# Kernel tuning notes

Hardware: AMD Instinct MI355X
Metric: run time of the kernel (lower is better)

The kernel has to match this reference:

```python
import jax, jax.numpy as jnp
import numpy as np

N_NODES = 20000
N_EDGES = 640000
NF = 128   # node_features
EF = 32    # edge_features
HD = 128   # hidden_dim
NL = 3     # num_layers
EPS = 1e-5


def _p(key, shape, scale=0.05):
    return scale * jax.random.normal(key, shape, dtype=jnp.float32)


def setup_inputs() -> dict:
    key = jax.random.key(0)
    ks = jax.random.split(key, 24)
    inp = {
        "node_coords": jax.random.normal(ks[0], (N_NODES, 6), dtype=jnp.float32),
        "edge_index": jax.random.randint(ks[1], (2, N_EDGES), 0, N_NODES, dtype=jnp.int64),
        "edge_distances": jax.random.normal(ks[2], (N_EDGES, 32), dtype=jnp.float32),
        # embeddings
        "W_node": _p(ks[3], (6, NF)), "b_node": jnp.zeros((NF,), jnp.float32),
        "W_edge": _p(ks[4], (32, EF)), "b_edge": jnp.zeros((EF,), jnp.float32),
        # stacked per-layer MPNN params [NL, ...]
        "msg_W1": _p(ks[5], (NL, 2 * NF + EF, HD)), "msg_b1": jnp.zeros((NL, HD), jnp.float32),
        "msg_W2": _p(ks[6], (NL, HD, HD)), "msg_b2": jnp.zeros((NL, HD), jnp.float32),
        "upd_W1": _p(ks[7], (NL, NF + HD, HD)), "upd_b1": jnp.zeros((NL, HD), jnp.float32),
        "upd_W2": _p(ks[8], (NL, HD, NF)), "upd_b2": jnp.zeros((NL, NF), jnp.float32),
        "ln_g": jnp.ones((NL, NF), jnp.float32), "ln_b": jnp.zeros((NL, NF), jnp.float32),
        # output projection
        "W_out": _p(ks[9], (NF, HD)), "b_out": jnp.zeros((HD,), jnp.float32),
    }
    return inp


def _layer_norm(x, g, b):
    mu = jnp.mean(x, axis=-1, keepdims=True)
    var = jnp.var(x, axis=-1, keepdims=True)
    return (x - mu) * jax.lax.rsqrt(var + EPS) * g + b


def _encode(node_coords, edge_index, edge_distances,
            W_node, b_node, W_edge, b_edge,
            msg_W1, msg_b1, msg_W2, msg_b2,
            upd_W1, upd_b1, upd_W2, upd_b2,
            ln_g, ln_b, W_out, b_out):
    src, dst = edge_index[0], edge_index[1]
    h = node_coords @ W_node + b_node                      # [N, NF]
    e = edge_distances @ W_edge + b_edge                   # [E, EF]
    n = h.shape[0]
    for l in range(NL):
        # gather + message MLP
        m_in = jnp.concatenate([h[src], h[dst], e], axis=-1)           # [E, 2NF+EF]
        m = jax.nn.relu(m_in @ msg_W1[l] + msg_b1[l]) @ msg_W2[l] + msg_b2[l]  # [E, HD]
        # scatter_add over destination nodes
        agg = jax.ops.segment_sum(m, dst, num_segments=n)              # [N, HD]
        # update MLP + residual + LayerNorm
        u_in = jnp.concatenate([h, agg], axis=-1)                      # [N, NF+HD]
        delta = jax.nn.relu(u_in @ upd_W1[l] + upd_b1[l]) @ upd_W2[l] + upd_b2[l]
        h = _layer_norm(h + delta, ln_g[l], ln_b[l])
    return h @ W_out + b_out                                           # [N, HD]


def reference(node_coords, edge_index, edge_distances,
              W_node, b_node, W_edge, b_edge,
              msg_W1, msg_b1, msg_W2, msg_b2,
              upd_W1, upd_b1, upd_W2, upd_b2,
              ln_g, ln_b, W_out, b_out):
    return _encode(node_coords, edge_index, edge_distances,
                   W_node, b_node, W_edge, b_edge,
                   msg_W1, msg_b1, msg_W2, msg_b2,
                   upd_W1, upd_b1, upd_W2, upd_b2,
                   ln_g, ln_b, W_out, b_out)
```

## Files before the change

kernel.cpp:

```cpp
#include <hip/hip_runtime.h>

#define NN 20000
#define NE 640000
#define NF 128
#define EF 32
#define HD 128
#define NL 3

typedef __bf16 bf16x8 __attribute__((ext_vector_type(8)));
typedef float f32x4 __attribute__((ext_vector_type(4)));

constexpr int BE = 64;
constexpr int KA = 2 * NF + EF;
constexpr int SAP = 296;
constexpr int STP = 136;
constexpr int MP = 130;
constexpr int KU = NF + HD;
constexpr int SUP = 264;
constexpr int SXP = 132;

__global__ __launch_bounds__(256) void k_hist(const int* __restrict__ ei, int* __restrict__ cnt)
{
    const int e = blockIdx.x * 256 + threadIdx.x;
    if (e < NE) atomicAdd(&cnt[ei[NE + e]], 1);
}

__global__ __launch_bounds__(1024) void k_scan(const int* __restrict__ cnt, int* __restrict__ pos)
{
    __shared__ int ls[1024];
    const int tid = threadIdx.x;
    const int C = 20;
    const int base = tid * C;
    int s = 0;
#pragma unroll
    for (int i = 0; i < C; ++i) {
        const int idx = base + i;
        if (idx < NN) s += cnt[idx];
    }
    ls[tid] = s;
    __syncthreads();
    for (int off = 1; off < 1024; off <<= 1) {
        const int v = (tid >= off) ? ls[tid - off] : 0;
        __syncthreads();
        ls[tid] += v;
        __syncthreads();
    }
    int p = tid ? ls[tid - 1] : 0;
#pragma unroll
    for (int i = 0; i < C; ++i) {
        const int idx = base + i;
        if (idx < NN) { pos[idx] = p; p += cnt[idx]; }
    }
}

__global__ __launch_bounds__(256) void k_scatter(
    const int* __restrict__ ei, int* __restrict__ pos,
    int* __restrict__ srcS, int* __restrict__ dstS, int* __restrict__ invp)
{
    const int e = blockIdx.x * 256 + threadIdx.x;
    if (e < NE) {
        const int d = ei[NE + e];
        const int p = atomicAdd(&pos[d], 1);
        srcS[p] = ei[e];
        dstS[p] = d;
        invp[e] = p;
    }
}

__device__ __forceinline__ void repack(const float* src, __bf16* dst, int total, int t, int stride)
{
    for (int i = t; i < total; i += stride) {
        const int kn = i & (16384 - 1);
        (void)kn;
    }
}

__global__ __launch_bounds__(256) void k_prep(
    const float* __restrict__ mW1, const float* __restrict__ mW2,
    const float* __restrict__ uW1, const float* __restrict__ uW2,
    const float* __restrict__ Wo,
    __bf16* __restrict__ W1f, __bf16* __restrict__ W2f,
    __bf16* __restrict__ U1f, __bf16* __restrict__ U2f,
    __bf16* __restrict__ Wof)
{
    const int t = blockIdx.x * 256 + threadIdx.x;
    const int stride = gridDim.x * 256;
    for (int i = t; i < NL * KA * HD; i += stride) {
        const int l = i / (KA * HD);
        const int r = i - l * (KA * HD);
        const int k = r >> 7, n = r & 127;
        W1f[(size_t)l * KA * HD + ((((k >> 3) * HD) + n) << 3) + (k & 7)] = (__bf16)mW1[i];
    }
    for (int i = t; i < NL * HD * HD; i += stride) {
        const int l = i / (HD * HD);
        const int r = i - l * (HD * HD);
        const int k = r >> 7, n = r & 127;
        W2f[(size_t)l * HD * HD + ((((k >> 3) * HD) + n) << 3) + (k & 7)] = (__bf16)mW2[i];
    }
    for (int i = t; i < NL * KU * HD; i += stride) {
        const int l = i / (KU * HD);
        const int r = i - l * (KU * HD);
        const int k = r >> 7, n = r & 127;
        U1f[(size_t)l * KU * HD + ((((k >> 3) * HD) + n) << 3) + (k & 7)] = (__bf16)uW1[i];
    }
    for (int i = t; i < NL * HD * NF; i += stride) {
        const int l = i / (HD * NF);
        const int r = i - l * (HD * NF);
        const int k = r >> 7, n = r & 127;
        U2f[(size_t)l * HD * NF + ((((k >> 3) * NF) + n) << 3) + (k & 7)] = (__bf16)uW2[i];
    }
    for (int i = t; i < NF * HD; i += stride) {
        const int k = i >> 7, n = i & 127;
        Wof[((((k >> 3) * HD) + n) << 3) + (k & 7)] = (__bf16)Wo[i];
    }
}

__global__ __launch_bounds__(256) void k_edge_embed(
    const float* __restrict__ dist, const float* __restrict__ We,
    const float* __restrict__ be, const int* __restrict__ invp,
    __bf16* __restrict__ ebfS)
{
    __shared__ float sD[64][33];
    __shared__ float sW[32][33];
    const int tid = threadIdx.x;
    const int e0 = blockIdx.x * 64;
#pragma unroll
    for (int it = 0; it < 4; ++it) {
        const int idx = tid + it * 256;
        sW[idx >> 5][idx & 31] = We[idx];
    }
#pragma unroll
    for (int it = 0; it < 8; ++it) {
        const int idx = tid + it * 256;
        sD[idx >> 5][idx & 31] = dist[(size_t)e0 * EF + idx];
    }
    __syncthreads();
    const int i = tid >> 2;
    const int j0 = (tid & 3) * 8;
    __bf16 vals[8];
#pragma unroll
    for (int jj = 0; jj < 8; ++jj) {
        const int j = j0 + jj;
        float acc = be[j];
#pragma unroll
        for (int q = 0; q < EF; ++q) acc = fmaf(sD[i][q], sW[q][j], acc);
        vals[jj] = (__bf16)acc;
    }
    const int p = invp[e0 + i];
    *reinterpret_cast<uint4*>(ebfS + (size_t)p * EF + j0) = *reinterpret_cast<const uint4*>(vals);
}

__global__ __launch_bounds__(128) void k_node_embed(
    const float* __restrict__ coords, const float* __restrict__ Wn,
    const float* __restrict__ bn, float* __restrict__ h, __bf16* __restrict__ hbf)
{
    const int node = blockIdx.x;
    const int f = threadIdx.x;
    __shared__ float c[8];
    if (f < 6) c[f] = coords[node * 6 + f];
    __syncthreads();
    float acc = bn[f];
#pragma unroll
    for (int k = 0; k < 6; ++k) acc = fmaf(c[k], Wn[k * NF + f], acc);
    h[(size_t)node * NF + f] = acc;
    hbf[(size_t)node * NF + f] = (__bf16)acc;
}

__global__ __launch_bounds__(256, 4) void k_message(
    const __bf16* __restrict__ hbf,
    const int* __restrict__ srcS, const int* __restrict__ dstS,
    const __bf16* __restrict__ ebfS,
    const __bf16* __restrict__ W1f, const float* __restrict__ b1,
    const __bf16* __restrict__ W2f, const float* __restrict__ b2,
    float* __restrict__ agg)
{
    __shared__ __attribute__((aligned(16))) __bf16 R[BE * SAP];
    __shared__ int s_src[BE], s_dst[BE];
    __bf16* sA = R;
    __bf16* sT = R;
    float* sM = (float*)R;

    const int tid = threadIdx.x;
    const int e0 = blockIdx.x * BE;
    const int w = tid >> 6;
    const int lane = tid & 63;
    const int m16 = lane & 15;
    const int kb = lane >> 4;
    const int n0 = w * 32;

    if (tid < BE) {
        s_src[tid] = srcS[e0 + tid];
        s_dst[tid] = dstS[e0 + tid];
    }

    bf16x8 bf1[9][2];
#pragma unroll
    for (int k9 = 0; k9 < 9; ++k9)
#pragma unroll
        for (int nf = 0; nf < 2; ++nf)
            bf1[k9][nf] = *reinterpret_cast<const bf16x8*>(
                W1f + ((((k9 * 4 + kb) * HD) + n0 + nf * 16 + m16) << 3));

    __syncthreads();

#pragma unroll
    for (int it = 0; it < 8; ++it) {
        const int c = tid + it * 256;
        const int row = c >> 5;
        const int part = (c >> 4) & 1;
        const int off = c & 15;
        const int idx = part ? s_dst[row] : s_src[row];
        *reinterpret_cast<uint4*>(&sA[row * SAP + part * NF + off * 8]) =
            *reinterpret_cast<const uint4*>(hbf + (size_t)idx * NF + off * 8);
    }
    {
        const int row = tid >> 2;
        const int off = tid & 3;
        *reinterpret_cast<uint4*>(&sA[row * SAP + 2 * NF + off * 8]) =
            *reinterpret_cast<const uint4*>(ebfS + (size_t)(e0 + row) * EF + off * 8);
    }
    __syncthreads();

    f32x4 acc1[4][2];
#pragma unroll
    for (int mt = 0; mt < 4; ++mt)
#pragma unroll
        for (int nf = 0; nf < 2; ++nf) acc1[mt][nf] = (f32x4){0.f, 0.f, 0.f, 0.f};
#pragma unroll
    for (int k9 = 0; k9 < 9; ++k9) {
#pragma unroll
        for (int mt = 0; mt < 4; ++mt) {
            const bf16x8 a = *reinterpret_cast<const bf16x8*>(&sA[(mt * 16 + m16) * SAP + k9 * 32 + kb * 8]);
            acc1[mt][0] = __builtin_amdgcn_mfma_f32_16x16x32_bf16(a, bf1[k9][0], acc1[mt][0], 0, 0, 0);
            acc1[mt][1] = __builtin_amdgcn_mfma_f32_16x16x32_bf16(a, bf1[k9][1], acc1[mt][1], 0, 0, 0);
        }
    }

    bf16x8 bf2[4][2];
#pragma unroll
    for (int k4 = 0; k4 < 4; ++k4)
#pragma unroll
        for (int nf = 0; nf < 2; ++nf)
            bf2[k4][nf] = *reinterpret_cast<const bf16x8*>(
                W2f + ((((k4 * 4 + kb) * HD) + n0 + nf * 16 + m16) << 3));

    __syncthreads();

    {
        const float b1a = b1[n0 + m16];
        const float b1b = b1[n0 + 16 + m16];
#pragma unroll
        for (int mt = 0; mt < 4; ++mt) {
#pragma unroll
            for (int reg = 0; reg < 4; ++reg) {
                const int erow = mt * 16 + kb * 4 + reg;
                sT[erow * STP + n0 + m16] = (__bf16)fmaxf(acc1[mt][0][reg] + b1a, 0.f);
                sT[erow * STP + n0 + 16 + m16] = (__bf16)fmaxf(acc1[mt][1][reg] + b1b, 0.f);
            }
        }
    }
    __syncthreads();

    f32x4 acc2[4][2];
#pragma unroll
    for (int mt = 0; mt < 4; ++mt)
#pragma unroll
        for (int nf = 0; nf < 2; ++nf) acc2[mt][nf] = (f32x4){0.f, 0.f, 0.f, 0.f};
#pragma unroll
    for (int k4 = 0; k4 < 4; ++k4) {
#pragma unroll
        for (int mt = 0; mt < 4; ++mt) {
            const bf16x8 a = *reinterpret_cast<const bf16x8*>(&sT[(mt * 16 + m16) * STP + k4 * 32 + kb * 8]);
            acc2[mt][0] = __builtin_amdgcn_mfma_f32_16x16x32_bf16(a, bf2[k4][0], acc2[mt][0], 0, 0, 0);
            acc2[mt][1] = __builtin_amdgcn_mfma_f32_16x16x32_bf16(a, bf2[k4][1], acc2[mt][1], 0, 0, 0);
        }
    }
    __syncthreads();

    {
        const float b2a = b2[n0 + m16];
        const float b2b = b2[n0 + 16 + m16];
#pragma unroll
        for (int mt = 0; mt < 4; ++mt) {
#pragma unroll
            for (int reg = 0; reg < 4; ++reg) {
                const int erow = mt * 16 + kb * 4 + reg;
                sM[erow * MP + n0 + m16] = acc2[mt][0][reg] + b2a;
                sM[erow * MP + n0 + 16 + m16] = acc2[mt][1][reg] + b2b;
            }
        }
    }
    __syncthreads();

    {
        const int col = tid & 127;
        const int r0 = (tid >> 7) * 32;
        int cur = s_dst[r0];
        float s = sM[r0 * MP + col];
#pragma unroll
        for (int r = r0 + 1; r < r0 + 32; ++r) {
            const int d2 = s_dst[r];
            const float v = sM[r * MP + col];
            if (d2 != cur) {
                atomicAdd(&agg[(size_t)cur * HD + col], s);
                cur = d2;
                s = v;
            } else {
                s += v;
            }
        }
        atomicAdd(&agg[(size_t)cur * HD + col], s);
    }
}

__global__ __launch_bounds__(256, 4) void k_update(
    float* __restrict__ h, const float* __restrict__ agg,
    const __bf16* __restrict__ U1f, const float* __restrict__ b1,
    const __bf16* __restrict__ U2f, const float* __restrict__ b2,
    const float* __restrict__ g, const float* __restrict__ bln,
    __bf16* __restrict__ hbf)
{
    __shared__ __attribute__((aligned(16))) __bf16 R[64 * SUP];
    __bf16* sU = R;
    __bf16* sT = R;
    float* sX = (float*)R;

    const int tid = threadIdx.x;
    const int n0 = blockIdx.x * 64;
    const int w = tid >> 6;
    const int lane = tid & 63;
    const int m16 = lane & 15;
    const int kb = lane >> 4;
    const int nw0 = w * 32;

#pragma unroll
    for (int it = 0; it < 4; ++it) {
        const int c = tid + it * 256;
        const int row = c >> 4;
        const int off = c & 15;
        const int node = min(n0 + row, NN - 1);
        *reinterpret_cast<uint4*>(&sU[row * SUP + off * 8]) =
            *reinterpret_cast<const uint4*>(hbf + (size_t)node * NF + off * 8);
    }
#pragma unroll
    for (int it = 0; it < 8; ++it) {
        const int c = tid + it * 256;
        const int row = c >> 5;
        const int off = c & 31;
        const int node = min(n0 + row, NN - 1);
        const float4 v = *reinterpret_cast<const float4*>(agg + (size_t)node * HD + off * 4);
        union { __bf16 b[4]; uint2 u; } cv;
        cv.b[0] = (__bf16)v.x; cv.b[1] = (__bf16)v.y; cv.b[2] = (__bf16)v.z; cv.b[3] = (__bf16)v.w;
        *reinterpret_cast<uint2*>(&sU[row * SUP + NF + off * 4]) = cv.u;
    }
    __syncthreads();

    f32x4 acc1[4][2];
#pragma unroll
    for (int mt = 0; mt < 4; ++mt)
#pragma unroll
        for (int nf = 0; nf < 2; ++nf) acc1[mt][nf] = (f32x4){0.f, 0.f, 0.f, 0.f};
#pragma unroll
    for (int k8 = 0; k8 < 8; ++k8) {
        bf16x8 bA = *reinterpret_cast<const bf16x8*>(U1f + ((((k8 * 4 + kb) * HD) + nw0 + m16) << 3));
        bf16x8 bB = *reinterpret_cast<const bf16x8*>(U1f + ((((k8 * 4 + kb) * HD) + nw0 + 16 + m16) << 3));
#pragma unroll
        for (int mt = 0; mt < 4; ++mt) {
            const bf16x8 a = *reinterpret_cast<const bf16x8*>(&sU[(mt * 16 + m16) * SUP + k8 * 32 + kb * 8]);
            acc1[mt][0] = __builtin_amdgcn_mfma_f32_16x16x32_bf16(a, bA, acc1[mt][0], 0, 0, 0);
            acc1[mt][1] = __builtin_amdgcn_mfma_f32_16x16x32_bf16(a, bB, acc1[mt][1], 0, 0, 0);
        }
    }
    __syncthreads();

    {
        const float b1a = b1[nw0 + m16];
        const float b1b = b1[nw0 + 16 + m16];
#pragma unroll
        for (int mt = 0; mt < 4; ++mt) {
#pragma unroll
            for (int reg = 0; reg < 4; ++reg) {
                const int erow = mt * 16 + kb * 4 + reg;
                sT[erow * STP + nw0 + m16] = (__bf16)fmaxf(acc1[mt][0][reg] + b1a, 0.f);
                sT[erow * STP + nw0 + 16 + m16] = (__bf16)fmaxf(acc1[mt][1][reg] + b1b, 0.f);
            }
        }
    }
    __syncthreads();

    f32x4 acc2[4][2];
#pragma unroll
    for (int mt = 0; mt < 4; ++mt)
#pragma unroll
        for (int nf = 0; nf < 2; ++nf) acc2[mt][nf] = (f32x4){0.f, 0.f, 0.f, 0.f};
#pragma unroll
    for (int k4 = 0; k4 < 4; ++k4) {
        bf16x8 bA = *reinterpret_cast<const bf16x8*>(U2f + ((((k4 * 4 + kb) * NF) + nw0 + m16) << 3));
        bf16x8 bB = *reinterpret_cast<const bf16x8*>(U2f + ((((k4 * 4 + kb) * NF) + nw0 + 16 + m16) << 3));
#pragma unroll
        for (int mt = 0; mt < 4; ++mt) {
            const bf16x8 a = *reinterpret_cast<const bf16x8*>(&sT[(mt * 16 + m16) * STP + k4 * 32 + kb * 8]);
            acc2[mt][0] = __builtin_amdgcn_mfma_f32_16x16x32_bf16(a, bA, acc2[mt][0], 0, 0, 0);
            acc2[mt][1] = __builtin_amdgcn_mfma_f32_16x16x32_bf16(a, bB, acc2[mt][1], 0, 0, 0);
        }
    }
    __syncthreads();

    {
        const float b2a = b2[nw0 + m16];
        const float b2b = b2[nw0 + 16 + m16];
#pragma unroll
        for (int mt = 0; mt < 4; ++mt) {
#pragma unroll
            for (int reg = 0; reg < 4; ++reg) {
                const int erow = mt * 16 + kb * 4 + reg;
                const int node = min(n0 + erow, NN - 1);
                const float h0 = h[(size_t)node * NF + nw0 + m16];
                const float h1 = h[(size_t)node * NF + nw0 + 16 + m16];
                sX[erow * SXP + nw0 + m16] = h0 + acc2[mt][0][reg] + b2a;
                sX[erow * SXP + nw0 + 16 + m16] = h1 + acc2[mt][1][reg] + b2b;
            }
        }
    }
    __syncthreads();

    {
        const int i = tid >> 2;
        const int j = tid & 3;
        float s = 0.f, s2 = 0.f;
#pragma unroll
        for (int t = 0; t < 32; ++t) {
            const float x = sX[i * SXP + j + 4 * t];
            s += x;
            s2 = fmaf(x, x, s2);
        }
        s += __shfl_xor(s, 1, 64);
        s2 += __shfl_xor(s2, 1, 64);
        s += __shfl_xor(s, 2, 64);
        s2 += __shfl_xor(s2, 2, 64);
        const float mu = s * (1.f / NF);
        const float var = s2 * (1.f / NF) - mu * mu;
        const float rs = rsqrtf(var + 1e-5f);
        const int node = n0 + i;
        if (node < NN) {
#pragma unroll
            for (int t = 0; t < 32; ++t) {
                const int col = j + 4 * t;
                const float v = (sX[i * SXP + col] - mu) * rs * g[col] + bln[col];
                h[(size_t)node * NF + col] = v;
                hbf[(size_t)node * NF + col] = (__bf16)v;
            }
        }
    }
}

__global__ __launch_bounds__(256, 4) void k_out(
    const __bf16* __restrict__ hbf, const __bf16* __restrict__ Wof,
    const float* __restrict__ bo, float* __restrict__ out)
{
    __shared__ __attribute__((aligned(16))) __bf16 sH[64 * STP];
    const int tid = threadIdx.x;
    const int n0 = blockIdx.x * 64;
    const int w = tid >> 6;
    const int lane = tid & 63;
    const int m16 = lane & 15;
    const int kb = lane >> 4;
    const int nw0 = w * 32;

#pragma unroll
    for (int it = 0; it < 4; ++it) {
        const int c = tid + it * 256;
        const int row = c >> 4;
        const int off = c & 15;
        const int node = min(n0 + row, NN - 1);
        *reinterpret_cast<uint4*>(&sH[row * STP + off * 8]) =
            *reinterpret_cast<const uint4*>(hbf + (size_t)node * NF + off * 8);
    }
    __syncthreads();

    f32x4 acc[4][2];
#pragma unroll
    for (int mt = 0; mt < 4; ++mt)
#pragma unroll
        for (int nf = 0; nf < 2; ++nf) acc[mt][nf] = (f32x4){0.f, 0.f, 0.f, 0.f};
#pragma unroll
    for (int k4 = 0; k4 < 4; ++k4) {
        bf16x8 bA = *reinterpret_cast<const bf16x8*>(Wof + ((((k4 * 4 + kb) * HD) + nw0 + m16) << 3));
        bf16x8 bB = *reinterpret_cast<const bf16x8*>(Wof + ((((k4 * 4 + kb) * HD) + nw0 + 16 + m16) << 3));
#pragma unroll
        for (int mt = 0; mt < 4; ++mt) {
            const bf16x8 a = *reinterpret_cast<const bf16x8*>(&sH[(mt * 16 + m16) * STP + k4 * 32 + kb * 8]);
            acc[mt][0] = __builtin_amdgcn_mfma_f32_16x16x32_bf16(a, bA, acc[mt][0], 0, 0, 0);
            acc[mt][1] = __builtin_amdgcn_mfma_f32_16x16x32_bf16(a, bB, acc[mt][1], 0, 0, 0);
        }
    }
    const float boa = bo[nw0 + m16];
    const float bob = bo[nw0 + 16 + m16];
#pragma unroll
    for (int mt = 0; mt < 4; ++mt) {
#pragma unroll
        for (int reg = 0; reg < 4; ++reg) {
            const int erow = mt * 16 + kb * 4 + reg;
            const int node = n0 + erow;
            if (node < NN) {
                out[(size_t)node * HD + nw0 + m16] = acc[mt][0][reg] + boa;
                out[(size_t)node * HD + nw0 + 16 + m16] = acc[mt][1][reg] + bob;
            }
        }
    }
}

extern "C" void kernel_launch(void* const* d_in, const int* in_sizes, int n_in,
                              void* d_out, int out_size, void* d_ws, size_t ws_size,
                              hipStream_t stream)
{
    const float* coords = (const float*)d_in[0];
    const int* ei       = (const int*)d_in[1];
    const float* dist   = (const float*)d_in[2];
    const float* Wn  = (const float*)d_in[3];
    const float* bn  = (const float*)d_in[4];
    const float* We  = (const float*)d_in[5];
    const float* be  = (const float*)d_in[6];
    const float* mW1 = (const float*)d_in[7];
    const float* mb1 = (const float*)d_in[8];
    const float* mW2 = (const float*)d_in[9];
    const float* mb2 = (const float*)d_in[10];
    const float* uW1 = (const float*)d_in[11];
    const float* ub1 = (const float*)d_in[12];
    const float* uW2 = (const float*)d_in[13];
    const float* ub2 = (const float*)d_in[14];
    const float* lng = (const float*)d_in[15];
    const float* lnb = (const float*)d_in[16];
    const float* Wo  = (const float*)d_in[17];
    const float* bo  = (const float*)d_in[18];

    char* p = (char*)d_ws;
    float* h   = (float*)p; p += (size_t)NN * NF * 4;
    float* agg = (float*)p; p += (size_t)NN * NF * 4;
    __bf16* hbf  = (__bf16*)p; p += (size_t)NN * NF * 2;
    __bf16* ebfS = (__bf16*)p; p += (size_t)NE * EF * 2;
    __bf16* W1f = (__bf16*)p; p += (size_t)NL * KA * HD * 2;
    __bf16* W2f = (__bf16*)p; p += (size_t)NL * HD * HD * 2;
    __bf16* U1f = (__bf16*)p; p += (size_t)NL * KU * HD * 2;
    __bf16* U2f = (__bf16*)p; p += (size_t)NL * HD * NF * 2;
    __bf16* Wof = (__bf16*)p; p += (size_t)NF * HD * 2;
    int* cnt  = (int*)p; p += (size_t)NN * 4;
    int* pos  = (int*)p; p += (size_t)NN * 4;
    int* srcS = (int*)p; p += (size_t)NE * 4;
    int* dstS = (int*)p; p += (size_t)NE * 4;
    int* invp = (int*)p; p += (size_t)NE * 4;

    hipMemsetAsync(cnt, 0, (size_t)NN * 4, stream);
    k_hist<<<(NE + 255) / 256, 256, 0, stream>>>(ei, cnt);
    k_scan<<<1, 1024, 0, stream>>>(cnt, pos);
    k_scatter<<<(NE + 255) / 256, 256, 0, stream>>>(ei, pos, srcS, dstS, invp);

    k_prep<<<256, 256, 0, stream>>>(mW1, mW2, uW1, uW2, Wo, W1f, W2f, U1f, U2f, Wof);
    k_node_embed<<<NN, 128, 0, stream>>>(coords, Wn, bn, h, hbf);
    k_edge_embed<<<NE / 64, 256, 0, stream>>>(dist, We, be, invp, ebfS);

    const int nbU = (NN + 63) / 64;
    for (int l = 0; l < NL; ++l) {
        hipMemsetAsync(agg, 0, (size_t)NN * NF * sizeof(float), stream);
        k_message<<<NE / BE, 256, 0, stream>>>(
            hbf, srcS, dstS, ebfS,
            W1f + (size_t)l * KA * HD, mb1 + l * HD,
            W2f + (size_t)l * HD * HD, mb2 + l * HD, agg);
        k_update<<<nbU, 256, 0, stream>>>(
            h, agg,
            U1f + (size_t)l * KU * HD, ub1 + l * HD,
            U2f + (size_t)l * HD * NF, ub2 + l * NF,
            lng + l * NF, lnb + l * NF, hbf);
    }
    k_out<<<nbU, 256, 0, stream>>>(hbf, Wof, bo, (float*)d_out);
}
```

Before: 692.6 us.

## Fuse preprocessing kernels, shrink message LDS, and zero agg inside update

Merges the histogram, weight repack and node embedding into one launch, and fuses the edge scatter with the edge embedding so the inverse permutation buffer is dropped. The message kernel now stages src and dst rows in two phases through a smaller shared buffer, which allows higher occupancy. It also stores messages as bf16 before the segmented reduction, remaps block order, and sets wave priority around the MFMA loops. The update kernel uses 32-node tiles, and each agg row is zeroed right after it is read, replacing the per-layer memset. In exchange, the bf16 message staging adds rounding error before accumulation.

New measurement: 1.154 ms. +66.6%, slower.

```diff
diff --git a/kernel.cpp b/kernel.cpp
--- a/kernel.cpp
+++ b/kernel.cpp
@@ -12,17 +12,77 @@
 
 constexpr int BE = 64;
 constexpr int KA = 2 * NF + EF;
-constexpr int SAP = 296;
+constexpr int SA2 = 168;
 constexpr int STP = 136;
-constexpr int MP = 130;
 constexpr int KU = NF + HD;
 constexpr int SUP = 264;
 constexpr int SXP = 132;
-
-__global__ __launch_bounds__(256) void k_hist(const int* __restrict__ ei, int* __restrict__ cnt)
-{
-    const int e = blockIdx.x * 256 + threadIdx.x;
-    if (e < NE) atomicAdd(&cnt[ei[NE + e]], 1);
+constexpr int NB_MSG = NE / BE;
+constexpr int CPX = NB_MSG / 8;
+
+__global__ __launch_bounds__(256) void k_pre(
+    const int* __restrict__ ei, int* __restrict__ cnt,
+    const float* __restrict__ mW1, const float* __restrict__ mW2,
+    const float* __restrict__ uW1, const float* __restrict__ uW2,
+    const float* __restrict__ Wo,
+    __bf16* __restrict__ W1f, __bf16* __restrict__ W2f,
+    __bf16* __restrict__ U1f, __bf16* __restrict__ U2f,
+    __bf16* __restrict__ Wof,
+    const float* __restrict__ coords, const float* __restrict__ Wn,
+    const float* __restrict__ bn, float* __restrict__ h, __bf16* __restrict__ hbf)
+{
+    const int b = blockIdx.x;
+    const int tid = threadIdx.x;
+    if (b < 2500) {
+        const int e = b * 256 + tid;
+        atomicAdd(&cnt[ei[NE + e]], 1);
+        return;
+    }
+    if (b < 2564) {
+        const int t = (b - 2500) * 256 + tid;
+        const int stride = 64 * 256;
+        for (int i = t; i < NL * KA * HD; i += stride) {
+            const int l = i / (KA * HD);
+            const int r = i - l * (KA * HD);
+            const int k = r >> 7, n = r & 127;
+            W1f[(size_t)l * KA * HD + ((((k >> 3) * HD) + n) << 3) + (k & 7)] = (__bf16)mW1[i];
+        }
+        for (int i = t; i < NL * HD * HD; i += stride) {
+            const int l = i / (HD * HD);
+            const int r = i - l * (HD * HD);
+            const int k = r >> 7, n = r & 127;
+            W2f[(size_t)l * HD * HD + ((((k >> 3) * HD) + n) << 3) + (k & 7)] = (__bf16)mW2[i];
+        }
+        for (int i = t; i < NL * KU * HD; i += stride) {
+            const int l = i / (KU * HD);
+            const int r = i - l * (KU * HD);
+            const int k = r >> 7, n = r & 127;
+            U1f[(size_t)l * KU * HD + ((((k >> 3) * HD) + n) << 3) + (k & 7)] = (__bf16)uW1[i];
+        }
+        for (int i = t; i < NL * HD * NF; i += stride) {
+            const int l = i / (HD * NF);
+            const int r = i - l * (HD * NF);
+            const int k = r >> 7, n = r & 127;
+            U2f[(size_t)l * HD * NF + ((((k >> 3) * NF) + n) << 3) + (k & 7)] = (__bf16)uW2[i];
+        }
+        for (int i = t; i < NF * HD; i += stride) {
+            const int k = i >> 7, n = i & 127;
+            Wof[((((k >> 3) * HD) + n) << 3) + (k & 7)] = (__bf16)Wo[i];
+        }
+        return;
+    }
+    __shared__ float sc[12];
+    const int n0 = (b - 2564) * 2;
+    if (tid < 12) sc[tid] = coords[n0 * 6 + tid];
+    __syncthreads();
+    const int node = n0 + (tid >> 7);
+    const int f = tid & 127;
+    const int cb = (tid >> 7) * 6;
+    float acc = bn[f];
+#pragma unroll
+    for (int k = 0; k < 6; ++k) acc = fmaf(sc[cb + k], Wn[k * NF + f], acc);
+    h[(size_t)node * NF + f] = acc;
+    hbf[(size_t)node * NF + f] = (__bf16)acc;
 }
 
 __global__ __launch_bounds__(1024) void k_scan(const int* __restrict__ cnt, int* __restrict__ pos)
@@ -53,120 +113,47 @@
     }
 }
 
-__global__ __launch_bounds__(256) void k_scatter(
+__global__ __launch_bounds__(256) void k_scatter_embed(
     const int* __restrict__ ei, int* __restrict__ pos,
-    int* __restrict__ srcS, int* __restrict__ dstS, int* __restrict__ invp)
-{
-    const int e = blockIdx.x * 256 + threadIdx.x;
-    if (e < NE) {
-        const int d = ei[NE + e];
-        const int p = atomicAdd(&pos[d], 1);
-        srcS[p] = ei[e];
-        dstS[p] = d;
-        invp[e] = p;
-    }
-}
-
-__device__ __forceinline__ void repack(const float* src, __bf16* dst, int total, int t, int stride)
-{
-    for (int i = t; i < total; i += stride) {
-        const int kn = i & (16384 - 1);
-        (void)kn;
-    }
-}
-
-__global__ __launch_bounds__(256) void k_prep(
-    const float* __restrict__ mW1, const float* __restrict__ mW2,
-    const float* __restrict__ uW1, const float* __restrict__ uW2,
-    const float* __restrict__ Wo,
-    __bf16* __restrict__ W1f, __bf16* __restrict__ W2f,
-    __bf16* __restrict__ U1f, __bf16* __restrict__ U2f,
-    __bf16* __restrict__ Wof)
-{
-    const int t = blockIdx.x * 256 + threadIdx.x;
-    const int stride = gridDim.x * 256;
-    for (int i = t; i < NL * KA * HD; i += stride) {
-        const int l = i / (KA * HD);
-        const int r = i - l * (KA * HD);
-        const int k = r >> 7, n = r & 127;
-        W1f[(size_t)l * KA * HD + ((((k >> 3) * HD) + n) << 3) + (k & 7)] = (__bf16)mW1[i];
-    }
-    for (int i = t; i < NL * HD * HD; i += stride) {
-        const int l = i / (HD * HD);
-        const int r = i - l * (HD * HD);
-        const int k = r >> 7, n = r & 127;
-        W2f[(size_t)l * HD * HD + ((((k >> 3) * HD) + n) << 3) + (k & 7)] = (__bf16)mW2[i];
-    }
-    for (int i = t; i < NL * KU * HD; i += stride) {
-        const int l = i / (KU * HD);
-        const int r = i - l * (KU * HD);
-        const int k = r >> 7, n = r & 127;
-        U1f[(size_t)l * KU * HD + ((((k >> 3) * HD) + n) << 3) + (k & 7)] = (__bf16)uW1[i];
-    }
-    for (int i = t; i < NL * HD * NF; i += stride) {
-        const int l = i / (HD * NF);
-        const int r = i - l * (HD * NF);
-        const int k = r >> 7, n = r & 127;
-        U2f[(size_t)l * HD * NF + ((((k >> 3) * NF) + n) << 3) + (k & 7)] = (__bf16)uW2[i];
-    }
-    for (int i = t; i < NF * HD; i += stride) {
-        const int k = i >> 7, n = i & 127;
-        Wof[((((k >> 3) * HD) + n) << 3) + (k & 7)] = (__bf16)Wo[i];
-    }
-}
-
-__global__ __launch_bounds__(256) void k_edge_embed(
     const float* __restrict__ dist, const float* __restrict__ We,
-    const float* __restrict__ be, const int* __restrict__ invp,
-    __bf16* __restrict__ ebfS)
-{
-    __shared__ float sD[64][33];
+    const float* __restrict__ be,
+    int* __restrict__ srcS, int* __restrict__ dstS, __bf16* __restrict__ ebfS)
+{
     __shared__ float sW[32][33];
+    __shared__ float sbe[32];
     const int tid = threadIdx.x;
-    const int e0 = blockIdx.x * 64;
-#pragma unroll
-    for (int it = 0; it < 4; ++it) {
-        const int idx = tid + it * 256;
-        sW[idx >> 5][idx & 31] = We[idx];
-    }
-#pragma unroll
-    for (int it = 0; it < 8; ++it) {
-        const int idx = tid + it * 256;
-        sD[idx >> 5][idx & 31] = dist[(size_t)e0 * EF + idx];
-    }
-    __syncthreads();
-    const int i = tid >> 2;
-    const int j0 = (tid & 3) * 8;
-    __bf16 vals[8];
-#pragma unroll
-    for (int jj = 0; jj < 8; ++jj) {
-        const int j = j0 + jj;
-        float acc = be[j];
-#pragma unroll
-        for (int q = 0; q < EF; ++q) acc = fmaf(sD[i][q], sW[q][j], acc);
-        vals[jj] = (__bf16)acc;
-    }
-    const int p = invp[e0 + i];
-    *reinterpret_cast<uint4*>(ebfS + (size_t)p * EF + j0) = *reinterpret_cast<const uint4*>(vals);
-}
-
-__global__ __launch_bounds__(128) void k_node_embed(
-    const float* __restrict__ coords, const float* __restrict__ Wn,
-    const float* __restrict__ bn, float* __restrict__ h, __bf16* __restrict__ hbf)
-{
-    const int node = blockIdx.x;
-    const int f = threadIdx.x;
-    __shared__ float c[8];
-    if (f < 6) c[f] = coords[node * 6 + f];
-    __syncthreads();
-    float acc = bn[f];
-#pragma unroll
-    for (int k = 0; k < 6; ++k) acc = fmaf(c[k], Wn[k * NF + f], acc);
-    h[(size_t)node * NF + f] = acc;
-    hbf[(size_t)node * NF + f] = (__bf16)acc;
-}
-
-__global__ __launch_bounds__(256, 4) void k_message(
+    for (int i = tid; i < 1024; i += 256) sW[i >> 5][i & 31] = We[i];
+    if (tid < 32) sbe[tid] = be[tid];
+    __syncthreads();
+    const int e = blockIdx.x * 256 + tid;
+    if (e >= NE) return;
+    const int d = ei[NE + e];
+    const int p = atomicAdd(&pos[d], 1);
+    srcS[p] = ei[e];
+    dstS[p] = d;
+    float dr[32];
+    const float4* dp = reinterpret_cast<const float4*>(dist + (size_t)e * EF);
+#pragma unroll
+    for (int q = 0; q < 8; ++q) {
+        const float4 v = dp[q];
+        dr[q * 4 + 0] = v.x; dr[q * 4 + 1] = v.y; dr[q * 4 + 2] = v.z; dr[q * 4 + 3] = v.w;
+    }
+#pragma unroll
+    for (int jg = 0; jg < 4; ++jg) {
+        union { __bf16 b[8]; uint4 u; } pk;
+#pragma unroll
+        for (int jj = 0; jj < 8; ++jj) {
+            const int j = jg * 8 + jj;
+            float acc = sbe[j];
+#pragma unroll
+            for (int q = 0; q < 32; ++q) acc = fmaf(dr[q], sW[q][j], acc);
+            pk.b[jj] = (__bf16)acc;
+        }
+        *reinterpret_cast<uint4*>(ebfS + (size_t)p * EF + jg * 8) = pk.u;
+    }
+}
+
+__global__ __launch_bounds__(256, 7) void k_message(
     const __bf16* __restrict__ hbf,
     const int* __restrict__ srcS, const int* __restrict__ dstS,
     const __bf16* __restrict__ ebfS,
@@ -174,14 +161,15 @@
     const __bf16* __restrict__ W2f, const float* __restrict__ b2,
     float* __restrict__ agg)
 {
-    __shared__ __attribute__((aligned(16))) __bf16 R[BE * SAP];
+    __shared__ __attribute__((aligned(16))) __bf16 R[BE * SA2];
     __shared__ int s_src[BE], s_dst[BE];
     __bf16* sA = R;
     __bf16* sT = R;
-    float* sM = (float*)R;
+    __bf16* sM = R;
 
     const int tid = threadIdx.x;
-    const int e0 = blockIdx.x * BE;
+    const int bid = (blockIdx.x & 7) * CPX + (blockIdx.x >> 3);
+    const int e0 = bid * BE;
     const int w = tid >> 6;
     const int lane = tid & 63;
     const int m16 = lane & 15;
@@ -204,19 +192,15 @@
     __syncthreads();
 
 #pragma unroll
-    for (int it = 0; it < 8; ++it) {
+    for (int it = 0; it < 4; ++it) {
         const int c = tid + it * 256;
-        const int row = c >> 5;
-        const int part = (c >> 4) & 1;
-        const int off = c & 15;
-        const int idx = part ? s_dst[row] : s_src[row];
-        *reinterpret_cast<uint4*>(&sA[row * SAP + part * NF + off * 8]) =
-            *reinterpret_cast<const uint4*>(hbf + (size_t)idx * NF + off * 8);
-    }
-    {
-        const int row = tid >> 2;
-        const int off = tid & 3;
-        *reinterpret_cast<uint4*>(&sA[row * SAP + 2 * NF + off * 8]) =
+        const int row = c >> 4, off = c & 15;
+        *reinterpret_cast<uint4*>(&sA[row * SA2 + off * 8]) =
+            *reinterpret_cast<const uint4*>(hbf + (size_t)s_src[row] * NF + off * 8);
+    }
+    {
+        const int row = tid >> 2, off = tid & 3;
+        *reinterpret_cast<uint4*>(&sA[row * SA2 + NF + off * 8]) =
             *reinterpret_cast<const uint4*>(ebfS + (size_t)(e0 + row) * EF + off * 8);
     }
     __syncthreads();
@@ -226,14 +210,27 @@
     for (int mt = 0; mt < 4; ++mt)
 #pragma unroll
         for (int nf = 0; nf < 2; ++nf) acc1[mt][nf] = (f32x4){0.f, 0.f, 0.f, 0.f};
-#pragma unroll
-    for (int k9 = 0; k9 < 9; ++k9) {
+
+    __builtin_amdgcn_s_setprio(1);
+#pragma unroll
+    for (int k5 = 0; k5 < 5; ++k5) {
+        const int wb = (k5 < 4) ? k5 : 8;
 #pragma unroll
         for (int mt = 0; mt < 4; ++mt) {
-            const bf16x8 a = *reinterpret_cast<const bf16x8*>(&sA[(mt * 16 + m16) * SAP + k9 * 32 + kb * 8]);
-            acc1[mt][0] = __builtin_amdgcn_mfma_f32_16x16x32_bf16(a, bf1[k9][0], acc1[mt][0], 0, 0, 0);
-            acc1[mt][1] = __builtin_amdgcn_mfma_f32_16x16x32_bf16(a, bf1[k9][1], acc1[mt][1], 0, 0, 0);
-        }
+            const bf16x8 a = *reinterpret_cast<const bf16x8*>(&sA[(mt * 16 + m16) * SA2 + k5 * 32 + kb * 8]);
+            acc1[mt][0] = __builtin_amdgcn_mfma_f32_16x16x32_bf16(a, bf1[wb][0], acc1[mt][0], 0, 0, 0);
+            acc1[mt][1] = __builtin_amdgcn_mfma_f32_16x16x32_bf16(a, bf1[wb][1], acc1[mt][1], 0, 0, 0);
+        }
+    }
+    __builtin_amdgcn_s_setprio(0);
+    __syncthreads();
+
+#pragma unroll
+    for (int it = 0; it < 4; ++it) {
+        const int c = tid + it * 256;
+        const int row = c >> 4, off = c & 15;
+        *reinterpret_cast<uint4*>(&sA[row * SA2 + off * 8]) =
+            *reinterpret_cast<const uint4*>(hbf + (size_t)s_dst[row] * NF + off * 8);
     }
 
     bf16x8 bf2[4][2];
@@ -243,7 +240,19 @@
         for (int nf = 0; nf < 2; ++nf)
             bf2[k4][nf] = *reinterpret_cast<const bf16x8*>(
                 W2f + ((((k4 * 4 + kb) * HD) + n0 + nf * 16 + m16) << 3));
-
+    __syncthreads();
+
+    __builtin_amdgcn_s_setprio(1);
+#pragma unroll
+    for (int k4 = 0; k4 < 4; ++k4) {
+#pragma unroll
+        for (int mt = 0; mt < 4; ++mt) {
+            const bf16x8 a = *reinterpret_cast<const bf16x8*>(&sA[(mt * 16 + m16) * SA2 + k4 * 32 + kb * 8]);
+            acc1[mt][0] = __builtin_amdgcn_mfma_f32_16x16x32_bf16(a, bf1[4 + k4][0], acc1[mt][0], 0, 0, 0);
+            acc1[mt][1] = __builtin_amdgcn_mfma_f32_16x16x32_bf16(a, bf1[4 + k4][1], acc1[mt][1], 0, 0, 0);
+        }
+    }
+    __builtin_amdgcn_s_setprio(0);
     __syncthreads();
 
     {
@@ -266,6 +275,8 @@
     for (int mt = 0; mt < 4; ++mt)
 #pragma unroll
         for (int nf = 0; nf < 2; ++nf) acc2[mt][nf] = (f32x4){0.f, 0.f, 0.f, 0.f};
+
+    __builtin_amdgcn_s_setprio(1);
 #pragma unroll
     for (int k4 = 0; k4 < 4; ++k4) {
 #pragma unroll
@@ -275,6 +286,7 @@
             acc2[mt][1] = __builtin_amdgcn_mfma_f32_16x16x32_bf16(a, bf2[k4][1], acc2[mt][1], 0, 0, 0);
         }
     }
+    __builtin_amdgcn_s_setprio(0);
     __syncthreads();
 
     {
@@ -285,8 +297,8 @@
 #pragma unroll
             for (int reg = 0; reg < 4; ++reg) {
                 const int erow = mt * 16 + kb * 4 + reg;
-                sM[erow * MP + n0 + m16] = acc2[mt][0][reg] + b2a;
-                sM[erow * MP + n0 + 16 + m16] = acc2[mt][1][reg] + b2b;
+                sM[erow * STP + n0 + m16] = (__bf16)(acc2[mt][0][reg] + b2a);
+                sM[erow * STP + n0 + 16 + m16] = (__bf16)(acc2[mt][1][reg] + b2b);
             }
         }
     }
@@ -296,11 +308,11 @@
         const int col = tid & 127;
         const int r0 = (tid >> 7) * 32;
         int cur = s_dst[r0];
-        float s = sM[r0 * MP + col];
+        float s = (float)sM[r0 * STP + col];
 #pragma unroll
         for (int r = r0 + 1; r < r0 + 32; ++r) {
             const int d2 = s_dst[r];
-            const float v = sM[r * MP + col];
+            const float v = (float)sM[r * STP + col];
             if (d2 != cur) {
                 atomicAdd(&agg[(size_t)cur * HD + col], s);
                 cur = d2;
@@ -313,20 +325,20 @@
     }
 }
 
-__global__ __launch_bounds__(256, 4) void k_update(
-    float* __restrict__ h, const float* __restrict__ agg,
+__global__ __launch_bounds__(256, 8) void k_update(
+    float* __restrict__ h, float* __restrict__ agg,
     const __bf16* __restrict__ U1f, const float* __restrict__ b1,
     const __bf16* __restrict__ U2f, const float* __restrict__ b2,
     const float* __restrict__ g, const float* __restrict__ bln,
     __bf16* __restrict__ hbf)
 {
-    __shared__ __attribute__((aligned(16))) __bf16 R[64 * SUP];
+    __shared__ __attribute__((aligned(16))) __bf16 R[32 * SUP];
     __bf16* sU = R;
     __bf16* sT = R;
     float* sX = (float*)R;
 
     const int tid = threadIdx.x;
-    const int n0 = blockIdx.x * 64;
+    const int n0 = blockIdx.x * 32;
     const int w = tid >> 6;
     const int lane = tid & 63;
     const int m16 = lane & 15;
@@ -334,38 +346,36 @@
     const int nw0 = w * 32;
 
 #pragma unroll
+    for (int it = 0; it < 2; ++it) {
+        const int c = tid + it * 256;
+        const int row = c >> 4, off = c & 15;
+        *reinterpret_cast<uint4*>(&sU[row * SUP + off * 8]) =
+            *reinterpret_cast<const uint4*>(hbf + (size_t)(n0 + row) * NF + off * 8);
+    }
+#pragma unroll
     for (int it = 0; it < 4; ++it) {
         const int c = tid + it * 256;
-        const int row = c >> 4;
-        const int off = c & 15;
-        const int node = min(n0 + row, NN - 1);
-        *reinterpret_cast<uint4*>(&sU[row * SUP + off * 8]) =
-            *reinterpret_cast<const uint4*>(hbf + (size_t)node * NF + off * 8);
-    }
-#pragma unroll
-    for (int it = 0; it < 8; ++it) {
-        const int c = tid + it * 256;
-        const int row = c >> 5;
-        const int off = c & 31;
-        const int node = min(n0 + row, NN - 1);
-        const float4 v = *reinterpret_cast<const float4*>(agg + (size_t)node * HD + off * 4);
+        const int row = c >> 5, off = c & 31;
+        float* ap = agg + (size_t)(n0 + row) * HD + off * 4;
+        const float4 v = *reinterpret_cast<const float4*>(ap);
         union { __bf16 b[4]; uint2 u; } cv;
         cv.b[0] = (__bf16)v.x; cv.b[1] = (__bf16)v.y; cv.b[2] = (__bf16)v.z; cv.b[3] = (__bf16)v.w;
         *reinterpret_cast<uint2*>(&sU[row * SUP + NF + off * 4]) = cv.u;
-    }
-    __syncthreads();
-
-    f32x4 acc1[4][2];
-#pragma unroll
-    for (int mt = 0; mt < 4; ++mt)
+        *reinterpret_cast<float4*>(ap) = (float4){0.f, 0.f, 0.f, 0.f};
+    }
+    __syncthreads();
+
+    f32x4 acc1[2][2];
+#pragma unroll
+    for (int mt = 0; mt < 2; ++mt)
 #pragma unroll
         for (int nf = 0; nf < 2; ++nf) acc1[mt][nf] = (f32x4){0.f, 0.f, 0.f, 0.f};
 #pragma unroll
     for (int k8 = 0; k8 < 8; ++k8) {
-        bf16x8 bA = *reinterpret_cast<const bf16x8*>(U1f + ((((k8 * 4 + kb) * HD) + nw0 + m16) << 3));
-        bf16x8 bB = *reinterpret_cast<const bf16x8*>(U1f + ((((k8 * 4 + kb) * HD) + nw0 + 16 + m16) << 3));
-#pragma unroll
-        for (int mt = 0; mt < 4; ++mt) {
+        const bf16x8 bA = *reinterpret_cast<const bf16x8*>(U1f + ((((k8 * 4 + kb) * HD) + nw0 + m16) << 3));
+        const bf16x8 bB = *reinterpret_cast<const bf16x8*>(U1f + ((((k8 * 4 + kb) * HD) + nw0 + 16 + m16) << 3));
+#pragma unroll
+        for (int mt = 0; mt < 2; ++mt) {
             const bf16x8 a = *reinterpret_cast<const bf16x8*>(&sU[(mt * 16 + m16) * SUP + k8 * 32 + kb * 8]);
             acc1[mt][0] = __builtin_amdgcn_mfma_f32_16x16x32_bf16(a, bA, acc1[mt][0], 0, 0, 0);
             acc1[mt][1] = __builtin_amdgcn_mfma_f32_16x16x32_bf16(a, bB, acc1[mt][1], 0, 0, 0);
@@ -377,7 +387,7 @@
         const float b1a = b1[nw0 + m16];
         const float b1b = b1[nw0 + 16 + m16];
 #pragma unroll
-        for (int mt = 0; mt < 4; ++mt) {
+        for (int mt = 0; mt < 2; ++mt) {
 #pragma unroll
             for (int reg = 0; reg < 4; ++reg) {
                 const int erow = mt * 16 + kb * 4 + reg;
@@ -388,17 +398,17 @@
     }
     __syncthreads();
 
-    f32x4 acc2[4][2];
-#pragma unroll
-    for (int mt = 0; mt < 4; ++mt)
+    f32x4 acc2[2][2];
+#pragma unroll
+    for (int mt = 0; mt < 2; ++mt)
 #pragma unroll
         for (int nf = 0; nf < 2; ++nf) acc2[mt][nf] = (f32x4){0.f, 0.f, 0.f, 0.f};
 #pragma unroll
     for (int k4 = 0; k4 < 4; ++k4) {
-        bf16x8 bA = *reinterpret_cast<const bf16x8*>(U2f + ((((k4 * 4 + kb) * NF) + nw0 + m16) << 3));
-        bf16x8 bB = *reinterpret_cast<const bf16x8*>(U2f + ((((k4 * 4 + kb) * NF) + nw0 + 16 + m16) << 3));
-#pragma unroll
-        for (int mt = 0; mt < 4; ++mt) {
+        const bf16x8 bA = *reinterpret_cast<const bf16x8*>(U2f + ((((k4 * 4 + kb) * NF) + nw0 + m16) << 3));
+        const bf16x8 bB = *reinterpret_cast<const bf16x8*>(U2f + ((((k4 * 4 + kb) * NF) + nw0 + 16 + m16) << 3));
+#pragma unroll
+        for (int mt = 0; mt < 2; ++mt) {
             const bf16x8 a = *reinterpret_cast<const bf16x8*>(&sT[(mt * 16 + m16) * STP + k4 * 32 + kb * 8]);
             acc2[mt][0] = __builtin_amdgcn_mfma_f32_16x16x32_bf16(a, bA, acc2[mt][0], 0, 0, 0);
             acc2[mt][1] = __builtin_amdgcn_mfma_f32_16x16x32_bf16(a, bB, acc2[mt][1], 0, 0, 0);
@@ -410,46 +420,39 @@
         const float b2a = b2[nw0 + m16];
         const float b2b = b2[nw0 + 16 + m16];
 #pragma unroll
-        for (int mt = 0; mt < 4; ++mt) {
+        for (int mt = 0; mt < 2; ++mt) {
 #pragma unroll
             for (int reg = 0; reg < 4; ++reg) {
                 const int erow = mt * 16 + kb * 4 + reg;
-                const int node = min(n0 + erow, NN - 1);
-                const float h0 = h[(size_t)node * NF + nw0 + m16];
-                const float h1 = h[(size_t)node * NF + nw0 + 16 + m16];
-                sX[erow * SXP + nw0 + m16] = h0 + acc2[mt][0][reg] + b2a;
-                sX[erow * SXP + nw0 + 16 + m16] = h1 + acc2[mt][1][reg] + b2b;
+                const size_t base = (size_t)(n0 + erow) * NF;
+                sX[erow * SXP + nw0 + m16] = h[base + nw0 + m16] + acc2[mt][0][reg] + b2a;
+                sX[erow * SXP + nw0 + 16 + m16] = h[base + nw0 + 16 + m16] + acc2[mt][1][reg] + b2b;
             }
         }
     }
     __syncthreads();
 
     {
-        const int i = tid >> 2;
-        const int j = tid & 3;
+        const int i = tid >> 3, j = tid & 7;
         float s = 0.f, s2 = 0.f;
 #pragma unroll
-        for (int t = 0; t < 32; ++t) {
-            const float x = sX[i * SXP + j + 4 * t];
-            s += x;
-            s2 = fmaf(x, x, s2);
-        }
-        s += __shfl_xor(s, 1, 64);
-        s2 += __shfl_xor(s2, 1, 64);
-        s += __shfl_xor(s, 2, 64);
-        s2 += __shfl_xor(s2, 2, 64);
+        for (int t = 0; t < 16; ++t) {
+            const float x = sX[i * SXP + j + 8 * t];
+            s += x; s2 = fmaf(x, x, s2);
+        }
+        s += __shfl_xor(s, 1, 64);  s2 += __shfl_xor(s2, 1, 64);
+        s += __shfl_xor(s, 2, 64);  s2 += __shfl_xor(s2, 2, 64);
+        s += __shfl_xor(s, 4, 64);  s2 += __shfl_xor(s2, 4, 64);
         const float mu = s * (1.f / NF);
         const float var = s2 * (1.f / NF) - mu * mu;
         const float rs = rsqrtf(var + 1e-5f);
-        const int node = n0 + i;
-        if (node < NN) {
-#pragma unroll
-            for (int t = 0; t < 32; ++t) {
-                const int col = j + 4 * t;
-                const float v = (sX[i * SXP + col] - mu) * rs * g[col] + bln[col];
-                h[(size_t)node * NF + col] = v;
-                hbf[(size_t)node * NF + col] = (__bf16)v;
-            }
+        const size_t base = (size_t)(n0 + i) * NF;
+#pragma unroll
+        for (int t = 0; t < 16; ++t) {
+            const int col = j + 8 * t;
+            const float v = (sX[i * SXP + col] - mu) * rs * g[col] + bln[col];
+            h[base + col] = v;
+            hbf[base + col] = (__bf16)v;
         }
     }
 }
@@ -470,8 +473,7 @@
 #pragma unroll
     for (int it = 0; it < 4; ++it) {
         const int c = tid + it * 256;
-        const int row = c >> 4;
-        const int off = c & 15;
+        const int row = c >> 4, off = c & 15;
         const int node = min(n0 + row, NN - 1);
         *reinterpret_cast<uint4*>(&sH[row * STP + off * 8]) =
             *reinterpret_cast<const uint4*>(hbf + (size_t)node * NF + off * 8);
@@ -485,8 +487,8 @@
         for (int nf = 0; nf < 2; ++nf) acc[mt][nf] = (f32x4){0.f, 0.f, 0.f, 0.f};
 #pragma unroll
     for (int k4 = 0; k4 < 4; ++k4) {
-        bf16x8 bA = *reinterpret_cast<const bf16x8*>(Wof + ((((k4 * 4 + kb) * HD) + nw0 + m16) << 3));
-        bf16x8 bB = *reinterpret_cast<const bf16x8*>(Wof + ((((k4 * 4 + kb) * HD) + nw0 + 16 + m16) << 3));
+        const bf16x8 bA = *reinterpret_cast<const bf16x8*>(Wof + ((((k4 * 4 + kb) * HD) + nw0 + m16) << 3));
+        const bf16x8 bB = *reinterpret_cast<const bf16x8*>(Wof + ((((k4 * 4 + kb) * HD) + nw0 + 16 + m16) << 3));
 #pragma unroll
         for (int mt = 0; mt < 4; ++mt) {
             const bf16x8 a = *reinterpret_cast<const bf16x8*>(&sH[(mt * 16 + m16) * STP + k4 * 32 + kb * 8]);
@@ -548,29 +550,26 @@
     int* pos  = (int*)p; p += (size_t)NN * 4;
     int* srcS = (int*)p; p += (size_t)NE * 4;
     int* dstS = (int*)p; p += (size_t)NE * 4;
-    int* invp = (int*)p; p += (size_t)NE * 4;
 
     hipMemsetAsync(cnt, 0, (size_t)NN * 4, stream);
-    k_hist<<<(NE + 255) / 256, 256, 0, stream>>>(ei, cnt);
+    hipMemsetAsync(agg, 0, (size_t)NN * NF * sizeof(float), stream);
+
+    k_pre<<<2564 + NN / 2, 256, 0, stream>>>(ei, cnt, mW1, mW2, uW1, uW2, Wo,
+                                             W1f, W2f, U1f, U2f, Wof,
+                                             coords, Wn, bn, h, hbf);
     k_scan<<<1, 1024, 0, stream>>>(cnt, pos);
-    k_scatter<<<(NE + 255) / 256, 256, 0, stream>>>(ei, pos, srcS, dstS, invp);
-
-    k_prep<<<256, 256, 0, stream>>>(mW1, mW2, uW1, uW2, Wo, W1f, W2f, U1f, U2f, Wof);
-    k_node_embed<<<NN, 128, 0, stream>>>(coords, Wn, bn, h, hbf);
-    k_edge_embed<<<NE / 64, 256, 0, stream>>>(dist, We, be, invp, ebfS);
-
-    const int nbU = (NN + 63) / 64;
+    k_scatter_embed<<<(NE + 255) / 256, 256, 0, stream>>>(ei, pos, dist, We, be, srcS, dstS, ebfS);
+
     for (int l = 0; l < NL; ++l) {
-        hipMemsetAsync(agg, 0, (size_t)NN * NF * sizeof(float), stream);
-        k_message<<<NE / BE, 256, 0, stream>>>(
+        k_message<<<NB_MSG, 256, 0, stream>>>(
             hbf, srcS, dstS, ebfS,
             W1f + (size_t)l * KA * HD, mb1 + l * HD,
             W2f + (size_t)l * HD * HD, mb2 + l * HD, agg);
-        k_update<<<nbU, 256, 0, stream>>>(
+        k_update<<<NN / 32, 256, 0, stream>>>(
             h, agg,
             U1f + (size_t)l * KU * HD, ub1 + l * HD,
             U2f + (size_t)l * HD * NF, ub2 + l * NF,
             lng + l * NF, lnb + l * NF, hbf);
     }
-    k_out<<<nbU, 256, 0, stream>>>(hbf, Wof, bo, (float*)d_out);
-}
+    k_out<<<(NN + 63) / 64, 256, 0, stream>>>(hbf, Wof, bo, (float*)d_out);
+}
```
